# Performance work log

Measured on AMD Instinct MI355X. Metric: run time of the kernel, lower is better.

Reference implementation:

```python
import jax, jax.numpy as jnp
import numpy as np

NUM_BOXES = 16384
NUM_CLASS = 3
CODE_SIZE = 7
NMS_PRE = 1024
NMS_POST = 512
NMS_THRESH = 0.8
EPS = 1e-8


def _cross(a, b):
    return a[..., 0] * b[..., 1] - a[..., 1] * b[..., 0]


def _bev_corners(b5):
    # b5: (..., 5) = (cx, cy, dx, dy, ry) -> corners (..., 4, 2)
    c, s = jnp.cos(b5[..., 4]), jnp.sin(b5[..., 4])
    off = jnp.array([[0.5, 0.5], [-0.5, 0.5], [-0.5, -0.5], [0.5, -0.5]], dtype=b5.dtype)
    lx = b5[..., 2:3] * off[:, 0]  # (..., 4)
    ly = b5[..., 3:4] * off[:, 1]
    cx = b5[..., 0:1] + lx * c[..., None] - ly * s[..., None]
    cy = b5[..., 1:2] + lx * s[..., None] + ly * c[..., None]
    return jnp.stack([cx, cy], axis=-1)


def _points_in_box(p, b5):
    # p: (..., K, 2), b5: (..., 5) -> (..., K) bool (point inside rotated rect)
    c, s = jnp.cos(b5[..., 4:5]), jnp.sin(b5[..., 4:5])
    rel = p - b5[..., None, 0:2]
    qx = rel[..., 0] * c + rel[..., 1] * s
    qy = -rel[..., 0] * s + rel[..., 1] * c
    return (jnp.abs(qx) <= b5[..., 2:3] * 0.5 + 1e-5) & (jnp.abs(qy) <= b5[..., 3:4] * 0.5 + 1e-5)


def _pairwise_bev_iou(b5):
    # b5: (N, 5) -> (N, N) rotated BEV IoU (matches iou3d nms_gpu's BEV IoU)
    a = b5[:, None, :]
    b = b5[None, :, :]
    ca = _bev_corners(a)  # (N,1,4,2)
    cb = _bev_corners(b)  # (1,N,4,2)
    # edge-edge segment intersections: (N,N,4,4)
    a0, da = ca, jnp.roll(ca, -1, axis=-2) - ca
    b0, db = cb, jnp.roll(cb, -1, axis=-2) - cb
    A0, DA = a0[..., :, None, :], da[..., :, None, :]
    B0, DB = b0[..., None, :, :], db[..., None, :, :]
    den = _cross(DA, DB)
    d = B0 - A0
    den_s = jnp.where(jnp.abs(den) > EPS, den, 1.0)
    t = _cross(d, DB) / den_s
    u = _cross(d, DA) / den_s
    ok = (jnp.abs(den) > EPS) & (t >= 0) & (t <= 1) & (u >= 0) & (u <= 1)
    p_ee = A0 + t[..., None] * DA  # (N,N,4,4,2)
    shp = p_ee.shape[:-3]
    p_ee = p_ee.reshape(shp + (16, 2))
    ok = ok.reshape(shp + (16,))
    in_b = _points_in_box(ca, b)  # corners of A inside B: (N,N,4)
    in_a = _points_in_box(cb, a)  # corners of B inside A: (N,N,4)
    pts = jnp.concatenate([p_ee,
                           jnp.broadcast_to(ca, shp + (4, 2)),
                           jnp.broadcast_to(cb, shp + (4, 2))], axis=-2)  # (N,N,24,2)
    msk = jnp.concatenate([ok, in_b, in_a], axis=-1)  # (N,N,24)
    # order candidate vertices by angle around centroid (intersection is convex)
    cnt = jnp.maximum(msk.sum(-1, keepdims=True), 1)
    ctr = (pts * msk[..., None]).sum(-2, keepdims=True) / cnt[..., None]  # (N,N,1,2)
    ang = jnp.arctan2(pts[..., 1] - ctr[..., 1], pts[..., 0] - ctr[..., 0])
    ang = jnp.where(msk, ang, 1e9)  # invalid points sorted to the end
    order = jnp.argsort(ang, axis=-1)
    pts_s = jnp.take_along_axis(pts, order[..., None], axis=-2)
    msk_s = jnp.take_along_axis(msk, order, axis=-1)
    first = pts_s[..., 0:1, :]
    poly = jnp.where(msk_s[..., None], pts_s, first)  # pad with first vertex (zero shoelace contribution)
    inter = 0.5 * jnp.abs(_cross(poly, jnp.roll(poly, -1, axis=-2)).sum(-1))
    area_a = a[..., 2] * a[..., 3]
    area_b = b[..., 2] * b[..., 3]
    return inter / jnp.maximum(area_a + area_b - inter, 1e-6)


def _greedy_nms(iou, thresh):
    n = iou.shape[0]
    idx = jnp.arange(n)

    def body(i, supp):
        alive = jnp.logical_not(supp[i])
        return supp | (alive & (iou[i] > thresh) & (idx > i))

    supp = jax.lax.fori_loop(0, n, body, jnp.zeros((n,), dtype=bool))
    return ~supp


def _select_one(box_preds, cls_preds):
    # box_preds: (M, 7), cls_preds: (M, C) -> padded selected indices + validity
    scores = jnp.max(cls_preds, axis=1)
    _, top_idx = jax.lax.top_k(scores, NMS_PRE)  # score-descending, like torch.topk
    bev = box_preds[top_idx][:, jnp.array([0, 1, 3, 4, 6])]  # (cx,cy,dx,dy,ry)
    iou = _pairwise_bev_iou(bev)
    keep = _greedy_nms(iou, NMS_THRESH)
    pri = jnp.where(keep, jnp.arange(NMS_PRE), 2 * NMS_PRE)
    pos = jnp.sort(pri)[:NMS_POST]  # kept positions in score order
    valid = pos < NMS_PRE
    sel = top_idx[jnp.minimum(pos, NMS_PRE - 1)]
    return sel, valid


def setup_inputs() -> dict:
    key = jax.random.key(0)
    k1, k2, k3, k4, k5 = jax.random.split(key, 5)
    B = 2
    xy = jax.random.uniform(k1, (B, NUM_BOXES, 2), minval=-50.0, maxval=50.0)
    z = jax.random.uniform(k2, (B, NUM_BOXES, 1), minval=-2.0, maxval=1.0)
    dims = jax.random.uniform(k3, (B, NUM_BOXES, 3), minval=1.0, maxval=5.0)
    ry = jax.random.uniform(k4, (B, NUM_BOXES, 1), minval=-np.pi, maxval=np.pi)
    batch_box_preds = jnp.concatenate([xy, z, dims, ry], axis=-1).astype(jnp.float32)
    batch_cls_preds = (jax.random.normal(k5, (B, NUM_BOXES, NUM_CLASS)) * 3.0).astype(jnp.float32)
    return {"batch_box_preds": batch_box_preds, "batch_cls_preds": batch_cls_preds}


def reference(batch_box_preds, batch_cls_preds):
    # RoIHeadTemplate.proposal_layer: per-sample max-score, class-agnostic NMS,
    # scatter into zero-padded (B, NMS_POST, ...) tensors.
    sel, valid = jax.vmap(_select_one)(batch_box_preds, batch_cls_preds)  # (B, NMS_POST)
    rois = jnp.take_along_axis(batch_box_preds, sel[..., None], axis=1)
    logits = jnp.take_along_axis(batch_cls_preds, sel[..., None], axis=1)
    labels = jnp.argmax(logits, axis=-1)
    scores = jnp.max(logits, axis=-1)
    v = valid[..., None]
    rois = jnp.where(v, rois, 0.0)
    logits = jnp.where(v, logits, 0.0)
    scores = jnp.where(valid, scores, 0.0)
    roi_labels = jnp.where(valid, labels, 0) + 1  # padded slots end up as 1, same as torch (zeros + 1)
    return rois, scores, roi_labels, logits
```

## Files before the change

kernel.cpp:

```cpp
#include <hip/hip_runtime.h>
#include <hip/hip_bf16.h>
#include <math.h>

#define NBOX   16384
#define NPRE   1024
#define NPOST  512
#define NMS_TH 0.8f
#define DEN_EPS 1e-8f
#define NCAND  2048
#define NBUCK  8192
#define WMAX   (1u << 20)

typedef unsigned long long ull;

__device__ __forceinline__ unsigned mono_f32(float a) {
  unsigned u = __float_as_uint(a);
  return (u & 0x80000000u) ? ~u : (u | 0x80000000u);
}

__global__ __launch_bounds__(1024) void k_hist(
    const float* __restrict__ cls, ull* __restrict__ cand,
    unsigned* __restrict__ candCount, unsigned* __restrict__ nz,
    ull* __restrict__ mask, unsigned* __restrict__ wcnt) {
  __shared__ unsigned hist[NBUCK];
  __shared__ unsigned ssum[1024];
  __shared__ unsigned thrT;
  __shared__ unsigned cnt;
  int b = blockIdx.x;
  int t = threadIdx.x;
  nz[b * NPRE + t] = 0u;
  ull* mb = mask + (size_t)b * NPRE * 16;
#pragma unroll
  for (int k = 0; k < 16; ++k) mb[k * 1024 + t] = 0ull;
  if (b == 0 && t == 0) wcnt[0] = 0u;
#pragma unroll
  for (int k = 0; k < NBUCK / 1024; ++k) hist[t + k * 1024] = 0u;
  if (t == 0) cnt = 0u;
  __syncthreads();

  ull key[16];
#pragma unroll
  for (int k = 0; k < 16; ++k) {
    int i = k * 1024 + t;
    const float* cc = cls + ((size_t)b * NBOX + i) * 3;
    float s = fmaxf(cc[0], fmaxf(cc[1], cc[2]));
    unsigned u = mono_f32(s);
    key[k] = ((ull)u << 14) | (ull)(16383 - i);
    atomicAdd(&hist[u >> 19], 1u);
  }
  __syncthreads();

  unsigned s8 = 0;
#pragma unroll
  for (int k = 0; k < 8; ++k) s8 += hist[t * 8 + k];
  ssum[t] = s8;
  __syncthreads();
  for (int off = 1; off < 1024; off <<= 1) {
    unsigned v = ssum[t] + ((t + off < 1024) ? ssum[t + off] : 0u);
    __syncthreads();
    ssum[t] = v;
    __syncthreads();
  }
  unsigned Sown = ssum[t];
  unsigned Snxt = (t < 1023) ? ssum[t + 1] : 0u;
  if (Sown >= NPRE && Snxt < NPRE) {
    unsigned c = Snxt;
    unsigned T = t * 8;
    for (int k = 7; k >= 0; --k) {
      c += hist[t * 8 + k];
      if (c >= NPRE) { T = t * 8 + k; break; }
    }
    thrT = T;
  }
  __syncthreads();
  unsigned T = thrT;
#pragma unroll
  for (int k = 0; k < 16; ++k) {
    unsigned bkt = (unsigned)(key[k] >> 33);
    if (bkt >= T) {
      unsigned pos = atomicAdd(&cnt, 1u);
      if (pos < NCAND) cand[(size_t)b * NCAND + pos] = key[k];
    }
  }
  __syncthreads();
  if (t == 0) candCount[b] = (cnt < NCAND) ? cnt : NCAND;
}

__global__ __launch_bounds__(256) void k_ranksel(
    const float* __restrict__ box, const ull* __restrict__ cand,
    const unsigned* __restrict__ candCount,
    int* __restrict__ topi, float* __restrict__ binfo) {
  __shared__ ull lk[NCAND];
  int b = blockIdx.y;
  int tid = threadIdx.x;
  int j = blockIdx.x * 256 + tid;
  unsigned C = candCount[b];
#pragma unroll
  for (int k = 0; k < NCAND / 256; ++k) {
    int idx = k * 256 + tid;
    lk[idx] = ((unsigned)idx < C) ? cand[(size_t)b * NCAND + idx] : 0ULL;
  }
  __syncthreads();
  ull my = ((unsigned)j < C) ? lk[j] : 0ULL;
  int r = 0;
  const ulonglong2* p2 = (const ulonglong2*)lk;
#pragma unroll 8
  for (int k = 0; k < NCAND / 2; ++k) {
    ulonglong2 kk = p2[k];
    r += (kk.x > my) ? 1 : 0;
    r += (kk.y > my) ? 1 : 0;
  }
  if ((unsigned)j >= C || r >= NPRE) return;
  int i = 16383 - (int)(my & 0x3FFFULL);
  topi[b * NPRE + r] = i;
  const float* bp = box + ((size_t)b * NBOX + i) * 7;
  float x = bp[0], y = bp[1], dx = bp[3], dy = bp[4], ry = bp[6];
  float c = cosf(ry), s = sinf(ry);
  float* o = binfo + ((size_t)b * NPRE + r) * 16;
  o[0] = x; o[1] = y; o[2] = dx; o[3] = dy; o[4] = c; o[5] = s;
  const float offx[4] = {0.5f, -0.5f, -0.5f, 0.5f};
  const float offy[4] = {0.5f, 0.5f, -0.5f, -0.5f};
#pragma unroll
  for (int k = 0; k < 4; ++k) {
    float lx = dx * offx[k], ly = dy * offy[k];
    o[6 + k]  = x + lx * c - ly * s;
    o[10 + k] = y + lx * s + ly * c;
  }
  o[14] = 0.5f * sqrtf(dx * dx + dy * dy);
  o[15] = dx * dy;
}

__device__ bool iou_exact_gt(const float* __restrict__ Ab, const float* __restrict__ Bb) {
  float ax = Ab[0], ay = Ab[1], bx = Bb[0], by = Bb[1];
  float aA = Ab[15], aB = Bb[15];
  float acx[4], acy[4], bcx[4], bcy[4];
#pragma unroll
  for (int k = 0; k < 4; ++k) {
    acx[k] = Ab[6 + k]; acy[k] = Ab[10 + k];
    bcx[k] = Bb[6 + k]; bcy[k] = Bb[10 + k];
  }
  float px[24], py[24];
  bool act[24];
#pragma unroll
  for (int p = 0; p < 4; ++p) {
    float A0x = acx[p], A0y = acy[p];
    float DAx = acx[(p + 1) & 3] - A0x, DAy = acy[(p + 1) & 3] - A0y;
#pragma unroll
    for (int q = 0; q < 4; ++q) {
      float B0x = bcx[q], B0y = bcy[q];
      float DBx = bcx[(q + 1) & 3] - B0x, DBy = bcy[(q + 1) & 3] - B0y;
      float den = DAx * DBy - DAy * DBx;
      float dxx = B0x - A0x, dyy = B0y - A0y;
      bool dok = fabsf(den) > DEN_EPS;
      float dens = dok ? den : 1.0f;
      float t = (dxx * DBy - dyy * DBx) / dens;
      float u = (dxx * DAy - dyy * DAx) / dens;
      int k = p * 4 + q;
      px[k] = A0x + t * DAx;
      py[k] = A0y + t * DAy;
      act[k] = dok && t >= 0.f && t <= 1.f && u >= 0.f && u <= 1.f;
    }
  }
  float cA = Ab[4], sA = Ab[5], cB = Bb[4], sB = Bb[5];
#pragma unroll
  for (int k = 0; k < 4; ++k) {
    float rx = acx[k] - bx, ry = acy[k] - by;
    float qx =  rx * cB + ry * sB, qy = -rx * sB + ry * cB;
    px[16 + k] = acx[k]; py[16 + k] = acy[k];
    act[16 + k] = (fabsf(qx) <= Bb[2] * 0.5f + 1e-5f) && (fabsf(qy) <= Bb[3] * 0.5f + 1e-5f);
  }
#pragma unroll
  for (int k = 0; k < 4; ++k) {
    float rx = bcx[k] - ax, ry = bcy[k] - ay;
    float qx =  rx * cA + ry * sA, qy = -rx * sA + ry * cA;
    px[20 + k] = bcx[k]; py[20 + k] = bcy[k];
    act[20 + k] = (fabsf(qx) <= Ab[2] * 0.5f + 1e-5f) && (fabsf(qy) <= Ab[3] * 0.5f + 1e-5f);
  }
  int cnt = 0; float sx = 0.f, sy = 0.f;
#pragma unroll
  for (int k = 0; k < 24; ++k)
    if (act[k]) { cnt++; sx += px[k]; sy += py[k]; }
  float fc = (float)(cnt > 1 ? cnt : 1);
  float cx0 = sx / fc, cy0 = sy / fc;
  ull key[24];
#pragma unroll
  for (int k = 0; k < 24; ++k) {
    float ang = atan2f(py[k] - cy0, px[k] - cx0);
    key[k] = act[k] ? ((((ull)mono_f32(ang)) << 5) | (ull)k) : ~0ull;
  }
  ull kmin = ~0ull; float fx = 0.f, fy = 0.f;
#pragma unroll
  for (int k = 0; k < 24; ++k) {
    bool lt = key[k] < kmin;
    kmin = lt ? key[k] : kmin;
    fx = lt ? px[k] : fx;
    fy = lt ? py[k] : fy;
  }
  float ssum = 0.f;
#pragma unroll
  for (int k = 0; k < 24; ++k) {
    ull myk = key[k];
    ull best = ~0ull; float nx = fx, ny = fy;
#pragma unroll
    for (int j = 0; j < 24; ++j) {
      bool c = (key[j] > myk) && (key[j] < best);
      best = c ? key[j] : best;
      nx = c ? px[j] : nx;
      ny = c ? py[j] : ny;
    }
    float contrib = px[k] * ny - py[k] * nx;
    ssum += (myk != ~0ull) ? contrib : 0.f;
  }
  float inter = 0.5f * fabsf(ssum);
  float uni = aA + aB - inter;
  return inter / fmaxf(uni, 1e-6f) > NMS_TH;
}

__global__ void k_pairs(const float* __restrict__ binfo, unsigned* __restrict__ wl,
                        unsigned* __restrict__ wcnt, unsigned wcap,
                        ull* __restrict__ mask, unsigned* __restrict__ nz) {
  int wv = (blockIdx.x * 256 + threadIdx.x) >> 6;
  int lane = threadIdx.x & 63;
  int w = wv & 15;
  int i = (wv >> 4) & (NPRE - 1);
  int b = wv >> 14;
  int j = w * 64 + lane;
  const float* base = binfo + (size_t)b * NPRE * 16;
  bool cand = false;
  if (w * 64 + 63 > i && j > i) {
    const float* Ab = base + (size_t)i * 16;
    const float* Bb = base + (size_t)j * 16;
    float ddx = Ab[0] - Bb[0], ddy = Ab[1] - Bb[1];
    float rr = Ab[14] + Bb[14] + 1e-3f;
    if (ddx * ddx + ddy * ddy <= rr * rr) {
      float aA = Ab[15], aB = Bb[15];
      float mn = fminf(aA, aB), mx = fmaxf(aA, aB);
      if (mn > NMS_TH * mx) cand = true;
    }
  }
  ull bal = __ballot(cand);
  if (!bal) return;
  unsigned baseOff = 0;
  if (lane == 0) baseOff = atomicAdd(wcnt, (unsigned)__popcll(bal));
  baseOff = (unsigned)__shfl((int)baseOff, 0, 64);
  if (cand) {
    unsigned off = baseOff + (unsigned)__popcll(bal & ((1ull << lane) - 1ull));
    if (off < wcap) {
      wl[off] = ((unsigned)b << 20) | ((unsigned)i << 10) | (unsigned)j;
    } else {
      if (iou_exact_gt(base + (size_t)i * 16, base + (size_t)j * 16)) {
        atomicOr(&mask[((size_t)b * NPRE + i) * 16 + w], 1ull << lane);
        atomicOr(&nz[b * NPRE + i], 1u << w);
      }
    }
  }
}

__global__ __launch_bounds__(256) void k_iou(
    const float* __restrict__ binfo, const unsigned* __restrict__ wl,
    const unsigned* __restrict__ wcnt, unsigned wcap,
    ull* __restrict__ mask, unsigned* __restrict__ nz) {
  unsigned n = wcnt[0];
  if (n > wcap) n = wcap;
  unsigned stride = gridDim.x * 256;
  for (unsigned t = blockIdx.x * 256 + threadIdx.x; t < n; t += stride) {
    unsigned pk = wl[t];
    unsigned b = pk >> 20, i = (pk >> 10) & 1023, j = pk & 1023;
    const float* base = binfo + (size_t)b * NPRE * 16;
    if (iou_exact_gt(base + (size_t)i * 16, base + (size_t)j * 16)) {
      atomicOr(&mask[((size_t)b * NPRE + i) * 16 + (j >> 6)], 1ull << (j & 63));
      atomicOr(&nz[b * NPRE + i], 1u << (j >> 6));
    }
  }
}

__global__ __launch_bounds__(64) void k_nms(const ull* __restrict__ mask,
                                            const unsigned* __restrict__ nz,
                                            ull* __restrict__ remv_out) {
  __shared__ ull rf[16];
  int b = blockIdx.x;
  int lane = threadIdx.x;
  for (int w = 0; w < 16; ++w) {
    unsigned v = nz[b * NPRE + w * 64 + lane];
    ull bb = __ballot(v != 0u);
    if (lane == 0) rf[w] = bb;
  }
  __syncthreads();
  ull remv = 0;
  for (int w = 0; w < 16; ++w) {
    ull bb = rf[w];
    while (bb) {
      int i = __ffsll(bb) - 1;
      bb &= bb - 1;
      int row = w * 64 + i;
      ull rw = __shfl(remv, w, 64);
      if (!((rw >> i) & 1ULL)) {
        unsigned nzi = nz[b * NPRE + row];
        ull m = 0;
        if (lane < 16 && ((nzi >> lane) & 1u))
          m = mask[((size_t)b * NPRE + row) * 16 + lane];
        remv |= m;
      }
    }
  }
  if (lane < 16) remv_out[b * 16 + lane] = remv;
}

__global__ __launch_bounds__(1024) void k_final(
    const float* __restrict__ box, const float* __restrict__ cls,
    const int* __restrict__ topi, const ull* __restrict__ remv,
    float* __restrict__ out, int B) {
  int b = blockIdx.x;
  int p = threadIdx.x;
  int lane = p & 63, wid = p >> 6;
  ull rw = remv[b * 16 + wid];
  int alive = ((rw >> lane) & 1ULL) ? 0 : 1;
  int v = alive;
#pragma unroll
  for (int off = 1; off < 64; off <<= 1) {
    int t = __shfl_up(v, off, 64);
    if (lane >= off) v += t;
  }
  __shared__ int wtot[16], woff[17];
  if (lane == 63) wtot[wid] = v;
  __syncthreads();
  if (p == 0) {
    int acc = 0;
    for (int t = 0; t < 16; ++t) { woff[t] = acc; acc += wtot[t]; }
    woff[16] = acc;
  }
  __syncthreads();
  int excl = v - alive + woff[wid];
  int total = woff[16];
  float* rois   = out;
  float* scores = out + (size_t)B * NPOST * 7;
  float* labels = scores + (size_t)B * NPOST;
  float* logits = labels + (size_t)B * NPOST;
  if (alive && excl < NPOST) {
    int s = excl;
    int orig = topi[b * NPRE + p];
    const float* bb = box + ((size_t)b * NBOX + orig) * 7;
    float* ro = rois + ((size_t)b * NPOST + s) * 7;
#pragma unroll
    for (int c = 0; c < 7; ++c) ro[c] = bb[c];
    const float* cc = cls + ((size_t)b * NBOX + orig) * 3;
    float l0 = cc[0], l1 = cc[1], l2 = cc[2];
    float m = fmaxf(l0, fmaxf(l1, l2));
    int lab = (l0 == m) ? 0 : ((l1 == m) ? 1 : 2);
    scores[b * NPOST + s] = m;
    labels[b * NPOST + s] = (float)(lab + 1);
    float* lg = logits + ((size_t)b * NPOST + s) * 3;
    lg[0] = l0; lg[1] = l1; lg[2] = l2;
  }
  if (p < NPOST && p >= total) {
    float* ro = rois + ((size_t)b * NPOST + p) * 7;
#pragma unroll
    for (int c = 0; c < 7; ++c) ro[c] = 0.f;
    scores[b * NPOST + p] = 0.f;
    labels[b * NPOST + p] = 1.f;
    float* lg = logits + ((size_t)b * NPOST + p) * 3;
    lg[0] = 0.f; lg[1] = 0.f; lg[2] = 0.f;
  }
}

extern "C" void kernel_launch(void* const* d_in, const int* in_sizes, int n_in,
                              void* d_out, int out_size, void* d_ws, size_t ws_size,
                              hipStream_t stream) {
  const float* box = (const float*)d_in[0];
  const float* cls = (const float*)d_in[1];
  float* out = (float*)d_out;
  int B = in_sizes[0] / (NBOX * 7);

  char* w = (char*)d_ws;
  size_t off = 0;
  ull* cand        = (ull*)(w + off);      off += (size_t)B * NCAND * sizeof(ull);
  unsigned* candCt = (unsigned*)(w + off); off += (size_t)B * sizeof(unsigned);
  int* topi        = (int*)(w + off);      off += (size_t)B * NPRE * sizeof(int);
  off = (off + 63) & ~(size_t)63;
  float* binfo     = (float*)(w + off);    off += (size_t)B * NPRE * 16 * sizeof(float);
  ull* mask        = (ull*)(w + off);      off += (size_t)B * NPRE * 16 * sizeof(ull);
  unsigned* nz     = (unsigned*)(w + off); off += (size_t)B * NPRE * sizeof(unsigned);
  ull* remv        = (ull*)(w + off);      off += (size_t)B * 16 * sizeof(ull);
  unsigned* wcnt   = (unsigned*)(w + off); off += 64;
  unsigned* wl     = (unsigned*)(w + off);
  unsigned wcap = 0;
  if (ws_size > off) {
    size_t rem = (ws_size - off) / sizeof(unsigned);
    wcap = (rem < (size_t)WMAX) ? (unsigned)rem : WMAX;
  }
  (void)out_size; (void)n_in;

  hipLaunchKernelGGL(k_hist,    dim3(B), dim3(1024), 0, stream, cls, cand, candCt, nz, mask, wcnt);
  hipLaunchKernelGGL(k_ranksel, dim3(NCAND / 256, B), dim3(256), 0, stream, box, cand, candCt, topi, binfo);
  hipLaunchKernelGGL(k_pairs,   dim3(B * NPRE * 16 / 4), dim3(256), 0, stream, binfo, wl, wcnt, wcap, mask, nz);
  hipLaunchKernelGGL(k_iou,     dim3(64), dim3(256), 0, stream, binfo, wl, wcnt, wcap, mask, nz);
  hipLaunchKernelGGL(k_nms,     dim3(B), dim3(64), 0, stream, mask, nz, remv);
  hipLaunchKernelGGL(k_final,   dim3(B), dim3(1024), 0, stream, box, cls, topi, remv, out, B);
}
```

Before: 143.2 us.

## Fuse IoU into pair filter, merge NMS into final, drop worklist

```diff
diff --git a/kernel.cpp b/kernel.cpp
--- a/kernel.cpp
+++ b/kernel.cpp
@@ -9,7 +9,6 @@
 #define DEN_EPS 1e-8f
 #define NCAND  2048
 #define NBUCK  8192
-#define WMAX   (1u << 20)
 
 typedef unsigned long long ull;
 
@@ -20,19 +19,15 @@
 
 __global__ __launch_bounds__(1024) void k_hist(
     const float* __restrict__ cls, ull* __restrict__ cand,
-    unsigned* __restrict__ candCount, unsigned* __restrict__ nz,
-    ull* __restrict__ mask, unsigned* __restrict__ wcnt) {
+    unsigned* __restrict__ candCount, unsigned* __restrict__ nz) {
   __shared__ unsigned hist[NBUCK];
-  __shared__ unsigned ssum[1024];
+  __shared__ unsigned wsuf[16];
   __shared__ unsigned thrT;
   __shared__ unsigned cnt;
   int b = blockIdx.x;
   int t = threadIdx.x;
+  int lane = t & 63, wv = t >> 6;
   nz[b * NPRE + t] = 0u;
-  ull* mb = mask + (size_t)b * NPRE * 16;
-#pragma unroll
-  for (int k = 0; k < 16; ++k) mb[k * 1024 + t] = 0ull;
-  if (b == 0 && t == 0) wcnt[0] = 0u;
 #pragma unroll
   for (int k = 0; k < NBUCK / 1024; ++k) hist[t + k * 1024] = 0u;
   if (t == 0) cnt = 0u;
@@ -53,16 +48,26 @@
   unsigned s8 = 0;
 #pragma unroll
   for (int k = 0; k < 8; ++k) s8 += hist[t * 8 + k];
-  ssum[t] = s8;
-  __syncthreads();
-  for (int off = 1; off < 1024; off <<= 1) {
-    unsigned v = ssum[t] + ((t + off < 1024) ? ssum[t + off] : 0u);
-    __syncthreads();
-    ssum[t] = v;
-    __syncthreads();
-  }
-  unsigned Sown = ssum[t];
-  unsigned Snxt = (t < 1023) ? ssum[t + 1] : 0u;
+  unsigned v = s8;
+#pragma unroll
+  for (int off = 1; off < 64; off <<= 1) {
+    unsigned o = __shfl_down(v, off, 64);
+    if (lane + off < 64) v += o;
+  }
+  if (lane == 0) wsuf[wv] = v;
+  __syncthreads();
+  if (t < 16) {
+    unsigned x = wsuf[t];
+#pragma unroll
+    for (int off = 1; off < 16; off <<= 1) {
+      unsigned o = __shfl_down(x, off, 64);
+      if (t + off < 16) x += o;
+    }
+    wsuf[t] = x;
+  }
+  __syncthreads();
+  unsigned Sown = v + ((wv < 15) ? wsuf[wv + 1] : 0u);
+  unsigned Snxt = Sown - s8;
   if (Sown >= NPRE && Snxt < NPRE) {
     unsigned c = Snxt;
     unsigned T = t * 8;
@@ -76,10 +81,16 @@
   unsigned T = thrT;
 #pragma unroll
   for (int k = 0; k < 16; ++k) {
-    unsigned bkt = (unsigned)(key[k] >> 33);
-    if (bkt >= T) {
-      unsigned pos = atomicAdd(&cnt, 1u);
-      if (pos < NCAND) cand[(size_t)b * NCAND + pos] = key[k];
+    bool c = (unsigned)(key[k] >> 33) >= T;
+    ull bal = __ballot(c);
+    if (bal) {
+      unsigned base = 0;
+      if (lane == 0) base = atomicAdd(&cnt, (unsigned)__popcll(bal));
+      base = (unsigned)__shfl((int)base, 0, 64);
+      if (c) {
+        unsigned pos = base + (unsigned)__popcll(bal & ((1ull << lane) - 1ull));
+        if (pos < NCAND) cand[(size_t)b * NCAND + pos] = key[k];
+      }
     }
   }
   __syncthreads();
@@ -89,7 +100,7 @@
 __global__ __launch_bounds__(256) void k_ranksel(
     const float* __restrict__ box, const ull* __restrict__ cand,
     const unsigned* __restrict__ candCount,
-    int* __restrict__ topi, float* __restrict__ binfo) {
+    int* __restrict__ topi, float* __restrict__ binfo, float4* __restrict__ pinfo) {
   __shared__ ull lk[NCAND];
   int b = blockIdx.y;
   int tid = threadIdx.x;
@@ -126,8 +137,10 @@
     o[6 + k]  = x + lx * c - ly * s;
     o[10 + k] = y + lx * s + ly * c;
   }
-  o[14] = 0.5f * sqrtf(dx * dx + dy * dy);
-  o[15] = dx * dy;
+  float rad = 0.5f * sqrtf(dx * dx + dy * dy);
+  float area = dx * dy;
+  o[14] = rad; o[15] = area;
+  pinfo[(size_t)b * NPRE + r] = make_float4(x, y, rad, area);
 }
 
 __device__ bool iou_exact_gt(const float* __restrict__ Ab, const float* __restrict__ Bb) {
@@ -216,104 +229,74 @@
   return inter / fmaxf(uni, 1e-6f) > NMS_TH;
 }
 
-__global__ void k_pairs(const float* __restrict__ binfo, unsigned* __restrict__ wl,
-                        unsigned* __restrict__ wcnt, unsigned wcap,
-                        ull* __restrict__ mask, unsigned* __restrict__ nz) {
+__global__ __launch_bounds__(256) void k_pairs(
+    const float* __restrict__ binfo, const float4* __restrict__ pinfo,
+    ull* __restrict__ mask, unsigned* __restrict__ nz) {
   int wv = (blockIdx.x * 256 + threadIdx.x) >> 6;
   int lane = threadIdx.x & 63;
   int w = wv & 15;
   int i = (wv >> 4) & (NPRE - 1);
   int b = wv >> 14;
+  if (w * 64 + 63 <= i) return;
   int j = w * 64 + lane;
+  float4 pj = pinfo[(size_t)b * NPRE + j];
+  float4 pi = pinfo[(size_t)b * NPRE + i];
+  bool cand = false;
+  if (j > i) {
+    float ddx = pi.x - pj.x, ddy = pi.y - pj.y;
+    float rr = pi.z + pj.z + 1e-3f;
+    if (ddx * ddx + ddy * ddy <= rr * rr) {
+      float mn = fminf(pi.w, pj.w), mx = fmaxf(pi.w, pj.w);
+      if (mn > NMS_TH * mx) cand = true;
+    }
+  }
   const float* base = binfo + (size_t)b * NPRE * 16;
-  bool cand = false;
-  if (w * 64 + 63 > i && j > i) {
-    const float* Ab = base + (size_t)i * 16;
-    const float* Bb = base + (size_t)j * 16;
-    float ddx = Ab[0] - Bb[0], ddy = Ab[1] - Bb[1];
-    float rr = Ab[14] + Bb[14] + 1e-3f;
-    if (ddx * ddx + ddy * ddy <= rr * rr) {
-      float aA = Ab[15], aB = Bb[15];
-      float mn = fminf(aA, aB), mx = fmaxf(aA, aB);
-      if (mn > NMS_TH * mx) cand = true;
-    }
-  }
-  ull bal = __ballot(cand);
-  if (!bal) return;
-  unsigned baseOff = 0;
-  if (lane == 0) baseOff = atomicAdd(wcnt, (unsigned)__popcll(bal));
-  baseOff = (unsigned)__shfl((int)baseOff, 0, 64);
-  if (cand) {
-    unsigned off = baseOff + (unsigned)__popcll(bal & ((1ull << lane) - 1ull));
-    if (off < wcap) {
-      wl[off] = ((unsigned)b << 20) | ((unsigned)i << 10) | (unsigned)j;
-    } else {
-      if (iou_exact_gt(base + (size_t)i * 16, base + (size_t)j * 16)) {
-        atomicOr(&mask[((size_t)b * NPRE + i) * 16 + w], 1ull << lane);
-        atomicOr(&nz[b * NPRE + i], 1u << w);
-      }
-    }
-  }
-}
-
-__global__ __launch_bounds__(256) void k_iou(
-    const float* __restrict__ binfo, const unsigned* __restrict__ wl,
-    const unsigned* __restrict__ wcnt, unsigned wcap,
-    ull* __restrict__ mask, unsigned* __restrict__ nz) {
-  unsigned n = wcnt[0];
-  if (n > wcap) n = wcap;
-  unsigned stride = gridDim.x * 256;
-  for (unsigned t = blockIdx.x * 256 + threadIdx.x; t < n; t += stride) {
-    unsigned pk = wl[t];
-    unsigned b = pk >> 20, i = (pk >> 10) & 1023, j = pk & 1023;
-    const float* base = binfo + (size_t)b * NPRE * 16;
-    if (iou_exact_gt(base + (size_t)i * 16, base + (size_t)j * 16)) {
-      atomicOr(&mask[((size_t)b * NPRE + i) * 16 + (j >> 6)], 1ull << (j & 63));
-      atomicOr(&nz[b * NPRE + i], 1u << (j >> 6));
-    }
-  }
-}
-
-__global__ __launch_bounds__(64) void k_nms(const ull* __restrict__ mask,
-                                            const unsigned* __restrict__ nz,
-                                            ull* __restrict__ remv_out) {
-  __shared__ ull rf[16];
-  int b = blockIdx.x;
-  int lane = threadIdx.x;
-  for (int w = 0; w < 16; ++w) {
-    unsigned v = nz[b * NPRE + w * 64 + lane];
-    ull bb = __ballot(v != 0u);
-    if (lane == 0) rf[w] = bb;
-  }
-  __syncthreads();
-  ull remv = 0;
-  for (int w = 0; w < 16; ++w) {
-    ull bb = rf[w];
-    while (bb) {
-      int i = __ffsll(bb) - 1;
-      bb &= bb - 1;
-      int row = w * 64 + i;
-      ull rw = __shfl(remv, w, 64);
-      if (!((rw >> i) & 1ULL)) {
-        unsigned nzi = nz[b * NPRE + row];
-        ull m = 0;
-        if (lane < 16 && ((nzi >> lane) & 1u))
-          m = mask[((size_t)b * NPRE + row) * 16 + lane];
-        remv |= m;
-      }
-    }
-  }
-  if (lane < 16) remv_out[b * 16 + lane] = remv;
+  bool pred = cand && iou_exact_gt(base + (size_t)i * 16, base + (size_t)j * 16);
+  ull bal = __ballot(pred);
+  if (lane == 0 && bal) {
+    mask[((size_t)b * NPRE + i) * 16 + w] = bal;
+    atomicOr(&nz[b * NPRE + i], 1u << w);
+  }
 }
 
 __global__ __launch_bounds__(1024) void k_final(
     const float* __restrict__ box, const float* __restrict__ cls,
-    const int* __restrict__ topi, const ull* __restrict__ remv,
-    float* __restrict__ out, int B) {
+    const int* __restrict__ topi, const ull* __restrict__ mask,
+    const unsigned* __restrict__ nz, float* __restrict__ out, int B) {
+  __shared__ ull remv_sh[16];
   int b = blockIdx.x;
   int p = threadIdx.x;
   int lane = p & 63, wid = p >> 6;
-  ull rw = remv[b * 16 + wid];
+
+  if (wid == 0) {
+    ull rfr[16];
+#pragma unroll
+    for (int w = 0; w < 16; ++w) {
+      unsigned vz = nz[b * NPRE + w * 64 + lane];
+      rfr[w] = __ballot(vz != 0u);
+    }
+    ull remv = 0;
+    for (int w = 0; w < 16; ++w) {
+      ull bb = rfr[w];
+      while (bb) {
+        int ii = __ffsll(bb) - 1;
+        bb &= bb - 1;
+        int row = w * 64 + ii;
+        ull rw = __shfl(remv, w, 64);
+        if (!((rw >> ii) & 1ULL)) {
+          unsigned nzi = nz[b * NPRE + row];
+          ull m = 0;
+          if (lane < 16 && ((nzi >> lane) & 1u))
+            m = mask[((size_t)b * NPRE + row) * 16 + lane];
+          remv |= m;
+        }
+      }
+    }
+    if (lane < 16) remv_sh[lane] = remv;
+  }
+  __syncthreads();
+
+  ull rw = remv_sh[wid];
   int alive = ((rw >> lane) & 1ULL) ? 0 : 1;
   int v = alive;
 #pragma unroll
@@ -378,22 +361,13 @@
   int* topi        = (int*)(w + off);      off += (size_t)B * NPRE * sizeof(int);
   off = (off + 63) & ~(size_t)63;
   float* binfo     = (float*)(w + off);    off += (size_t)B * NPRE * 16 * sizeof(float);
+  float4* pinfo    = (float4*)(w + off);   off += (size_t)B * NPRE * sizeof(float4);
   ull* mask        = (ull*)(w + off);      off += (size_t)B * NPRE * 16 * sizeof(ull);
   unsigned* nz     = (unsigned*)(w + off); off += (size_t)B * NPRE * sizeof(unsigned);
-  ull* remv        = (ull*)(w + off);      off += (size_t)B * 16 * sizeof(ull);
-  unsigned* wcnt   = (unsigned*)(w + off); off += 64;
-  unsigned* wl     = (unsigned*)(w + off);
-  unsigned wcap = 0;
-  if (ws_size > off) {
-    size_t rem = (ws_size - off) / sizeof(unsigned);
-    wcap = (rem < (size_t)WMAX) ? (unsigned)rem : WMAX;
-  }
-  (void)out_size; (void)n_in;
-
-  hipLaunchKernelGGL(k_hist,    dim3(B), dim3(1024), 0, stream, cls, cand, candCt, nz, mask, wcnt);
-  hipLaunchKernelGGL(k_ranksel, dim3(NCAND / 256, B), dim3(256), 0, stream, box, cand, candCt, topi, binfo);
-  hipLaunchKernelGGL(k_pairs,   dim3(B * NPRE * 16 / 4), dim3(256), 0, stream, binfo, wl, wcnt, wcap, mask, nz);
-  hipLaunchKernelGGL(k_iou,     dim3(64), dim3(256), 0, stream, binfo, wl, wcnt, wcap, mask, nz);
-  hipLaunchKernelGGL(k_nms,     dim3(B), dim3(64), 0, stream, mask, nz, remv);
-  hipLaunchKernelGGL(k_final,   dim3(B), dim3(1024), 0, stream, box, cls, topi, remv, out, B);
-}
+  (void)off; (void)ws_size; (void)out_size; (void)n_in;
+
+  hipLaunchKernelGGL(k_hist,    dim3(B), dim3(1024), 0, stream, cls, cand, candCt, nz);
+  hipLaunchKernelGGL(k_ranksel, dim3(NCAND / 256, B), dim3(256), 0, stream, box, cand, candCt, topi, binfo, pinfo);
+  hipLaunchKernelGGL(k_pairs,   dim3(B * NPRE * 16 / 4), dim3(256), 0, stream, binfo, pinfo, mask, nz);
+  hipLaunchKernelGGL(k_final,   dim3(B), dim3(1024), 0, stream, box, cls, topi, mask, nz, out, B);
+}
```

Measured after the change: 157.7 us. 10.1% more time.
